# Kernel optimization log

Hardware: AMD Instinct MI355X
Metric: run time of the kernel (lower is better)

## Reference

```python
import jax, jax.numpy as jnp
import numpy as np

TOP_K = 48
NUM_RBF = 16
MAX_REL = 32  # max_relative_feature
B, L = 2, 3072

# atom order in stacked tensor: N=0, Ca=1, C=2, O=3, Cb=4
_PAIRS = np.array([
    (0, 0), (2, 2), (3, 3), (4, 4), (1, 0), (1, 2), (1, 3), (1, 4),
    (0, 2), (0, 3), (0, 4), (4, 2), (4, 3), (3, 2), (0, 1), (2, 1),
    (3, 1), (4, 1), (2, 0), (3, 0), (4, 0), (2, 4), (3, 4), (2, 3)], dtype=np.int32)


def _rbf(D):
    # D [..., ] -> [..., NUM_RBF]
    mu = jnp.linspace(2.0, 22.0, NUM_RBF)
    sigma = (22.0 - 2.0) / NUM_RBF
    return jnp.exp(-(((D[..., None] - mu) / sigma) ** 2))


def setup_inputs() -> dict:
    key = jax.random.key(0)
    ks = jax.random.split(key, 8)
    X = jax.random.normal(ks[0], (B, L, 4, 3), dtype=jnp.float32) * 3.0
    mask = jnp.ones((B, L), dtype=jnp.float32)
    R_idx = jnp.sort(jax.random.randint(ks[1], (B, L), 0, 6144), axis=-1)
    chain_labels = jax.random.randint(ks[2], (B, L), 0, 4)
    pos_W = jax.random.normal(ks[3], (2 * MAX_REL + 2, 16), dtype=jnp.float32) * 0.1
    pos_b = jax.random.normal(ks[4], (16,), dtype=jnp.float32) * 0.02
    edge_W = jax.random.normal(ks[5], (16 + 25 * NUM_RBF, 128), dtype=jnp.float32) * 0.05
    ln_gamma = jnp.ones((128,), dtype=jnp.float32)
    ln_beta = jnp.zeros((128,), dtype=jnp.float32)
    return {"X": X, "mask": mask, "R_idx": R_idx, "chain_labels": chain_labels,
            "pos_W": pos_W, "pos_b": pos_b, "edge_W": edge_W,
            "ln_gamma": ln_gamma, "ln_beta": ln_beta}


def reference(X, mask, R_idx, chain_labels, pos_W, pos_b, edge_W, ln_gamma, ln_beta):
    # virtual Cb construction
    bvec = X[:, :, 1, :] - X[:, :, 0, :]
    cvec = X[:, :, 2, :] - X[:, :, 1, :]
    avec = jnp.cross(bvec, cvec)
    Ca = X[:, :, 1, :]
    Cb = -0.58273431 * avec + 0.56802827 * bvec - 0.54067466 * cvec + Ca
    atoms = jnp.stack([X[:, :, 0, :], Ca, X[:, :, 2, :], X[:, :, 3, :], Cb], axis=2)  # [B,L,5,3]

    # masked pairwise Ca distances + k smallest neighbors
    mask2d = mask[:, :, None] * mask[:, None, :]                        # [B,L,L]
    dX = Ca[:, :, None, :] - Ca[:, None, :, :]
    D = mask2d * jnp.sqrt(jnp.sum(dX ** 2, axis=-1) + 1e-6)
    D_max = jnp.max(D, axis=-1, keepdims=True)
    D_adjust = D + (1.0 - mask2d) * D_max
    k = min(TOP_K, X.shape[1])
    neg_vals, E_idx = jax.lax.top_k(-D_adjust, k)                       # [B,L,K]
    D_neighbors = -neg_vals

    # gather neighbor atom coords once: [B,L,K,5,3]
    atoms_nb = jax.vmap(lambda a, i: a[i])(atoms, E_idx)

    # 24 remaining atom-pair distances, restricted to neighbors (same math as
    # full cdist + gather since dist is computed per (i, E_idx[i,j]) pair)
    ai, bi = _PAIRS[:, 0], _PAIRS[:, 1]
    diff = atoms[:, :, None, ai, :] - atoms_nb[:, :, :, bi, :]          # [B,L,K,24,3]
    D24 = jnp.sqrt(jnp.sum(diff ** 2, axis=-1) + 1e-6)                  # [B,L,K,24]

    D_all = jnp.concatenate([D_neighbors[..., None], D24], axis=-1)    # [B,L,K,25]
    RBF_all = _rbf(D_all).reshape(D_all.shape[:3] + (25 * NUM_RBF,))   # [B,L,K,400]

    # positional encodings on neighbor offsets
    offset = R_idx[:, :, None] - R_idx[:, None, :]
    offset = jnp.take_along_axis(offset, E_idx, axis=2)                 # [B,L,K]
    same_chain = (chain_labels[:, :, None] - chain_labels[:, None, :] == 0).astype(jnp.int32)
    E_chains = jnp.take_along_axis(same_chain, E_idx, axis=2)           # [B,L,K]
    d = jnp.clip(offset + MAX_REL, 0, 2 * MAX_REL) * E_chains + (1 - E_chains) * (2 * MAX_REL + 1)
    E_positional = pos_W[d] + pos_b                                     # one-hot @ W == row gather

    E = jnp.concatenate([E_positional, RBF_all], axis=-1)              # [B,L,K,416]
    E = E @ edge_W                                                      # [B,L,K,128]
    mu = jnp.mean(E, axis=-1, keepdims=True)
    var = jnp.mean((E - mu) ** 2, axis=-1, keepdims=True)
    E = (E - mu) / jnp.sqrt(var + 1e-5) * ln_gamma + ln_beta
    return E, E_idx
```

## Files before the change

### kernel.cpp

```cpp
#include <hip/hip_runtime.h>
#include <hip/hip_bf16.h>
#include <stdint.h>
#include <math.h>

#define B_   2
#define L_   3072
#define K_   48
#define FDIM 416
#define NOUT 128
#define FRS8 424

__device__ const unsigned char PAIRC[24] = {
    0, 18, 27, 36, 8, 10, 11, 12, 2, 3, 4, 34, 35, 26,
    1, 17, 25, 33, 16, 24, 32, 20, 28, 19
};

typedef __attribute__((ext_vector_type(4))) float f32x4;

__global__ __launch_bounds__(256) void k_prep(const float* __restrict__ X,
                                              const float* __restrict__ edgeW,
                                              float* __restrict__ atoms,
                                              float* __restrict__ CaA,
                                              unsigned char* __restrict__ Wt8)
{
    const int bid = blockIdx.x;
    if (bid < 52) {
        int idx4 = bid * 256 + threadIdx.x;
        int b = idx4 * 4;
        int lhi = (b >> 3) & 3;
        int l15 = (b >> 5) & 15;
        int nt  = (b >> 9) & 7;
        int kt  = b >> 12;
        int n = nt * 16 + l15;
        int kbase = kt * 32 + lhi * 8 + (b & 7);
        float v0 = edgeW[(kbase + 0) * NOUT + n];
        float v1 = edgeW[(kbase + 1) * NOUT + n];
        float v2 = edgeW[(kbase + 2) * NOUT + n];
        float v3 = edgeW[(kbase + 3) * NOUT + n];
        int w = __builtin_amdgcn_cvt_pk_fp8_f32(v0, v1, 0, false);
        w = __builtin_amdgcn_cvt_pk_fp8_f32(v2, v3, w, true);
        ((unsigned int*)Wt8)[idx4] = (unsigned int)w;
    } else {
        int row = (bid - 52) * 256 + threadIdx.x;
        if (row >= B_ * L_) return;
        const float* x = X + row * 12;
        float nx = x[0], ny = x[1], nz = x[2];
        float cax = x[3], cay = x[4], caz = x[5];
        float cx = x[6], cy = x[7], cz = x[8];
        float ox = x[9], oy = x[10], oz = x[11];
        float bx = cax - nx, by = cay - ny, bz = caz - nz;
        float vx = cx - cax, vy = cy - cay, vz = cz - caz;
        float axv = by * vz - bz * vy;
        float ayv = bz * vx - bx * vz;
        float azv = bx * vy - by * vx;
        float cbx = -0.58273431f * axv + 0.56802827f * bx - 0.54067466f * vx + cax;
        float cby = -0.58273431f * ayv + 0.56802827f * by - 0.54067466f * vy + cay;
        float cbz = -0.58273431f * azv + 0.56802827f * bz - 0.54067466f * vz + caz;
        float* A = atoms + row * 16;
        A[0] = nx;  A[1] = ny;  A[2] = nz;
        A[3] = cax; A[4] = cay; A[5] = caz;
        A[6] = cx;  A[7] = cy;  A[8] = cz;
        A[9] = ox;  A[10] = oy; A[11] = oz;
        A[12] = cbx; A[13] = cby; A[14] = cbz;
        A[15] = 0.f;
        CaA[row * 3 + 0] = cax;
        CaA[row * 3 + 1] = cay;
        CaA[row * 3 + 2] = caz;
    }
}

__global__ __launch_bounds__(256) void k_topk(const float* __restrict__ CaA,
                                              const float* __restrict__ mask,
                                              int* __restrict__ eidx,
                                              float* __restrict__ dnb,
                                              float* __restrict__ out_eidx_f)
{
    __shared__ __align__(16) unsigned int SH[3072];
    unsigned int* hist  = SH;
    unsigned int* candJ = SH + 2048;
    unsigned long long* candK = (unsigned long long*)SH;
    __shared__ unsigned int swave[4];
    __shared__ int sP;
    __shared__ unsigned int sCnt;

    const int row = blockIdx.x;
    const int b = row / L_;
    const int tid = threadIdx.x;
    const int lane = tid & 63;
    const int wv = tid >> 6;

    #pragma unroll
    for (int i = 0; i < 8; ++i) hist[tid + 256 * i] = 0;
    if (tid == 0) sCnt = 0;

    const float caxf = CaA[row * 3 + 0];
    const float cayf = CaA[row * 3 + 1];
    const float cazf = CaA[row * 3 + 2];
    const float mif = mask[row];
    const float* Cb = CaA + (size_t)b * L_ * 3;
    const float* mb = mask + (size_t)b * L_;
    __syncthreads();

    unsigned int bits[12];
    #pragma unroll
    for (int m = 0; m < 12; ++m) {
        int j = tid + 256 * m;
        float dx = caxf - Cb[j * 3 + 0];
        float dy = cayf - Cb[j * 3 + 1];
        float dz = cazf - Cb[j * 3 + 2];
        float s = fmaf(dz, dz, fmaf(dy, dy, dx * dx)) + 1e-6f;
        float dist = sqrtf(s);
        bool live = (mif * mb[j]) != 0.0f;
        bits[m] = live ? __float_as_uint(dist) : 0x7F800000u;
        atomicAdd(&hist[bits[m] >> 20], 1u);
    }
    __syncthreads();

    unsigned int loc[8];
    unsigned int s = 0;
    #pragma unroll
    for (int i = 0; i < 8; ++i) { loc[i] = hist[tid * 8 + i]; s += loc[i]; }
    unsigned int sc = s;
    #pragma unroll
    for (int off = 1; off < 64; off <<= 1) {
        unsigned int o = __shfl_up(sc, off);
        if (lane >= off) sc += o;
    }
    if (lane == 63) swave[wv] = sc;
    __syncthreads();
    unsigned int base = 0;
    #pragma unroll
    for (int w = 0; w < 4; ++w) if (w < wv) base += swave[w];
    unsigned int cum = base + sc - s;
    #pragma unroll
    for (int i = 0; i < 8; ++i) {
        unsigned int c = loc[i];
        if (cum < K_ && cum + c >= K_) sP = tid * 8 + i;
        cum += c;
    }
    __syncthreads();
    const unsigned int Pth = (unsigned int)sP + 2;

    #pragma unroll
    for (int m = 0; m < 12; ++m) {
        if ((bits[m] >> 20) <= Pth) {
            unsigned int pos = atomicAdd(&sCnt, 1u);
            if (pos < 1024) candJ[pos] = (unsigned)(tid + 256 * m);
        }
    }
    __syncthreads();
    int cnt = (int)sCnt;
    if (cnt > 1024) cnt = 1024;

    const double cax = (double)caxf, cay = (double)cayf, caz = (double)cazf;
    for (int i = tid; i < cnt; i += 256) {
        int j = (int)candJ[i];
        double dx = cax - (double)Cb[j * 3 + 0];
        double dy = cay - (double)Cb[j * 3 + 1];
        double dz = caz - (double)Cb[j * 3 + 2];
        double ss = dx * dx;
        ss = ss + dy * dy;
        ss = ss + dz * dz;
        ss = ss + 1e-6;
        float v = (float)sqrt(ss);
        candK[i] = ((unsigned long long)__float_as_uint(v) << 32) | (unsigned)j;
    }
    __syncthreads();

    if (cnt <= 64) {
        if (wv == 0) {
            unsigned long long k = (lane < cnt) ? candK[lane] : ~0ull;
            #pragma unroll
            for (int size = 2; size <= 64; size <<= 1) {
                #pragma unroll
                for (int stride = size >> 1; stride >= 1; stride >>= 1) {
                    unsigned long long o = __shfl_xor(k, stride);
                    bool low = (lane & stride) == 0;
                    bool up = (lane & size) == 0 || size == 64;
                    unsigned long long mn = k < o ? k : o;
                    unsigned long long mx = k < o ? o : k;
                    k = (low == up) ? mn : mx;
                }
            }
            if (lane < K_) {
                int gj = (int)(unsigned)(k & 0xffffffffu);
                eidx[row * K_ + lane] = gj;
                dnb[row * K_ + lane] = __uint_as_float((unsigned)(k >> 32));
                out_eidx_f[row * K_ + lane] = (float)gj;
            }
        }
    } else {
        int M2 = 128;
        while (M2 < cnt) M2 <<= 1;
        for (int i = cnt + tid; i < M2; i += 256) candK[i] = ~0ull;
        for (int size = 2; size <= M2; size <<= 1) {
            for (int stride = size >> 1; stride > 0; stride >>= 1) {
                __syncthreads();
                for (int i = tid; i < M2; i += 256) {
                    int p = i ^ stride;
                    if (p > i) {
                        unsigned long long a = candK[i];
                        unsigned long long c2 = candK[p];
                        bool up = ((i & size) == 0);
                        if ((a > c2) == up) { candK[i] = c2; candK[p] = a; }
                    }
                }
            }
        }
        __syncthreads();
        if (tid < K_) {
            unsigned long long g = candK[tid];
            int gj = (int)(unsigned)(g & 0xffffffffu);
            eidx[row * K_ + tid] = gj;
            dnb[row * K_ + tid] = __uint_as_float((unsigned)(g >> 32));
            out_eidx_f[row * K_ + tid] = (float)gj;
        }
    }
}

__global__ __launch_bounds__(256) void k_edge(const float* __restrict__ atoms,
                                              const int* __restrict__ eidx,
                                              const float* __restrict__ dnb,
                                              const int* __restrict__ Ridx,
                                              const int* __restrict__ chain,
                                              const float* __restrict__ posW,
                                              const float* __restrict__ posb,
                                              const unsigned char* __restrict__ Wt8,
                                              const float* __restrict__ gamma,
                                              const float* __restrict__ beta,
                                              float* __restrict__ Eout)
{
    __shared__ __align__(16) unsigned char F8[K_ * FRS8];
    __shared__ __align__(16) float sAtoms[K_][16];
    __shared__ __align__(16) float sOwn[16];
    __shared__ int   sE[K_];
    __shared__ float sDnb[K_];
    __shared__ int   sDpos[K_];
    __shared__ float Psum[K_][4];
    __shared__ float Psq[K_][4];

    const int row = blockIdx.x;
    const int b = row / L_;
    const int tid = threadIdx.x;

    if (tid < K_) {
        sE[tid] = eidx[row * K_ + tid];
        sDnb[tid] = dnb[row * K_ + tid];
    }
    __syncthreads();

    if (tid < 192) {
        int k = tid >> 2, part = tid & 3;
        const float4 v = *(const float4*)(atoms + ((size_t)b * L_ + sE[k]) * 16 + part * 4);
        *(float4*)(&sAtoms[k][part * 4]) = v;
    } else if (tid < 196) {
        int part = tid - 192;
        *(float4*)(&sOwn[part * 4]) = *(const float4*)(atoms + (size_t)row * 16 + part * 4);
    } else if (tid >= 208) {
        int k = tid - 208;
        int j = sE[k];
        int off = Ridx[row] - Ridx[b * L_ + j];
        int ch = (chain[row] == chain[b * L_ + j]) ? 1 : 0;
        sDpos[k] = ch ? min(max(off + 32, 0), 64) : 65;
    }
    __syncthreads();

    if (tid < 240) {
        const int k = tid / 5;
        const int dd0 = tid - k * 5;
        unsigned char* Fk = F8 + k * FRS8;
        #pragma unroll
        for (int s5 = 0; s5 < 5; ++s5) {
            const int dd = dd0 + 5 * s5;
            float D;
            if (dd == 0) {
                D = sDnb[k];
            } else {
                int pr = PAIRC[dd - 1];
                int ai = pr >> 3, bi = pr & 7;
                float dx = sOwn[ai * 3 + 0] - sAtoms[k][bi * 3 + 0];
                float dy = sOwn[ai * 3 + 1] - sAtoms[k][bi * 3 + 1];
                float dz = sOwn[ai * 3 + 2] - sAtoms[k][bi * 3 + 2];
                D = sqrtf(fmaf(dz, dz, fmaf(dy, dy, dx * dx)) + 1e-6f);
            }
            float t = fminf((D - 2.0f) * 0.8f, 20.0f);
            unsigned int u[4];
            #pragma unroll
            for (int gp = 0; gp < 4; ++gp) {
                float e0 = __expf(-(t * t));
                float r  = __expf(fmaf(2.1333334f, t, -1.1377778f));
                float e1 = e0 * r; r *= 0.1027400f;
                float e2 = e1 * r; r *= 0.1027400f;
                float e3 = e2 * r;
                int w = __builtin_amdgcn_cvt_pk_fp8_f32(e0, e1, 0, false);
                w = __builtin_amdgcn_cvt_pk_fp8_f32(e2, e3, w, true);
                u[gp] = (unsigned int)w;
                t -= 4.2666667f;
            }
            unsigned char* dst = Fk + 16 + dd * 16;
            *(uint2*)(dst)     = make_uint2(u[0], u[1]);
            *(uint2*)(dst + 8) = make_uint2(u[2], u[3]);
        }
    }
    for (int s2 = tid; s2 < K_ * 16; s2 += 256) {
        int k = s2 >> 4, r = s2 & 15;
        float v = posW[sDpos[k] * 16 + r] + posb[r];
        int w = __builtin_amdgcn_cvt_pk_fp8_f32(v, v, 0, false);
        F8[k * FRS8 + r] = (unsigned char)(w & 0xff);
    }
    __syncthreads();

    const int lane = tid & 63;
    const int wv = tid >> 6;
    const int l15 = lane & 15;
    const int lhi = lane >> 4;

    f32x4 acc[3][2];
    #pragma unroll
    for (int mt = 0; mt < 3; ++mt)
        #pragma unroll
        for (int nn = 0; nn < 2; ++nn)
            acc[mt][nn] = (f32x4){0.f, 0.f, 0.f, 0.f};

    const unsigned char* wp = Wt8 + wv * 1024 + l15 * 32 + lhi * 8;
    long bc0 = *(const long*)(wp);
    long bc1 = *(const long*)(wp + 512);

    #pragma unroll 1
    for (int kt = 0; kt < 13; ++kt) {
        long bn0 = 0, bn1 = 0;
        if (kt < 12) {
            bn0 = *(const long*)(wp + (kt + 1) * 4096);
            bn1 = *(const long*)(wp + (kt + 1) * 4096 + 512);
        }
        const int k0 = kt * 32 + lhi * 8;
        long a0 = *(const long*)(F8 + (l15) * FRS8 + k0);
        long a1 = *(const long*)(F8 + (16 + l15) * FRS8 + k0);
        long a2 = *(const long*)(F8 + (32 + l15) * FRS8 + k0);
        acc[0][0] = __builtin_amdgcn_mfma_f32_16x16x32_fp8_fp8(a0, bc0, acc[0][0], 0, 0, 0);
        acc[0][1] = __builtin_amdgcn_mfma_f32_16x16x32_fp8_fp8(a0, bc1, acc[0][1], 0, 0, 0);
        acc[1][0] = __builtin_amdgcn_mfma_f32_16x16x32_fp8_fp8(a1, bc0, acc[1][0], 0, 0, 0);
        acc[1][1] = __builtin_amdgcn_mfma_f32_16x16x32_fp8_fp8(a1, bc1, acc[1][1], 0, 0, 0);
        acc[2][0] = __builtin_amdgcn_mfma_f32_16x16x32_fp8_fp8(a2, bc0, acc[2][0], 0, 0, 0);
        acc[2][1] = __builtin_amdgcn_mfma_f32_16x16x32_fp8_fp8(a2, bc1, acc[2][1], 0, 0, 0);
        bc0 = bn0;
        bc1 = bn1;
    }

    #pragma unroll
    for (int mt = 0; mt < 3; ++mt) {
        #pragma unroll
        for (int r = 0; r < 4; ++r) {
            float v0 = acc[mt][0][r], v1 = acc[mt][1][r];
            float sv = v0 + v1;
            float q = v0 * v0 + v1 * v1;
            #pragma unroll
            for (int off = 1; off < 16; off <<= 1) {
                sv += __shfl_xor(sv, off);
                q += __shfl_xor(q, off);
            }
            if (l15 == 0) {
                int er = mt * 16 + lhi * 4 + r;
                Psum[er][wv] = sv;
                Psq[er][wv] = q;
            }
        }
    }
    __syncthreads();

    const int c0 = wv * 32 + l15;
    float g2[2], be2[2];
    g2[0] = gamma[c0];      g2[1] = gamma[c0 + 16];
    be2[0] = beta[c0];      be2[1] = beta[c0 + 16];

    #pragma unroll
    for (int mt = 0; mt < 3; ++mt) {
        #pragma unroll
        for (int r = 0; r < 4; ++r) {
            int er = mt * 16 + lhi * 4 + r;
            float sv = Psum[er][0] + Psum[er][1] + Psum[er][2] + Psum[er][3];
            float q = Psq[er][0] + Psq[er][1] + Psq[er][2] + Psq[er][3];
            float mu = sv * (1.0f / 128.0f);
            float var = q * (1.0f / 128.0f) - mu * mu;
            float inv = 1.0f / sqrtf(var + 1e-5f);
            float* op = Eout + ((size_t)row * K_ + er) * 128;
            op[c0]      = (acc[mt][0][r] - mu) * inv * g2[0] + be2[0];
            op[c0 + 16] = (acc[mt][1][r] - mu) * inv * g2[1] + be2[1];
        }
    }
}

extern "C" void kernel_launch(void* const* d_in, const int* in_sizes, int n_in,
                              void* d_out, int out_size, void* d_ws, size_t ws_size,
                              hipStream_t stream) {
    const float* X     = (const float*)d_in[0];
    const float* mask  = (const float*)d_in[1];
    const int*   Ridx  = (const int*)d_in[2];
    const int*   chain = (const int*)d_in[3];
    const float* posW  = (const float*)d_in[4];
    const float* posb  = (const float*)d_in[5];
    const float* edgeW = (const float*)d_in[6];
    const float* gamma = (const float*)d_in[7];
    const float* beta  = (const float*)d_in[8];

    float* out   = (float*)d_out;
    float* Eout  = out;
    float* EidxF = out + (size_t)B_ * L_ * K_ * NOUT;

    float* atoms = (float*)d_ws;
    float* CaA   = atoms + (size_t)B_ * L_ * 16;
    int*   eidx  = (int*)(CaA + (size_t)B_ * L_ * 3);
    float* dnb   = (float*)(eidx + (size_t)B_ * L_ * K_);
    unsigned char* Wt8 = (unsigned char*)(dnb + (size_t)B_ * L_ * K_);

    hipLaunchKernelGGL(k_prep, dim3(52 + (B_ * L_ + 255) / 256), dim3(256), 0, stream,
                       X, edgeW, atoms, CaA, Wt8);
    hipLaunchKernelGGL(k_topk, dim3(B_ * L_), dim3(256), 0, stream,
                       CaA, mask, eidx, dnb, EidxF);
    hipLaunchKernelGGL(k_edge, dim3(B_ * L_), dim3(256), 0, stream,
                       atoms, eidx, dnb, Ridx, chain, posW, posb, Wt8, gamma, beta, Eout);
}
```

Measured before the change: 135.7 us.

## Replace per-edge RBF exponentials with quantized distance LUT and pack Ca with mask

Builds a 1920-entry table of FP8-packed RBF vectors, indexed by distance at 1/64 spacing, inside the prep kernel. The edge kernel then does one 16-byte table load per distance instead of computing exponentials. Ca coordinates and the mask are also packed into float4 so the top-k kernel reads each neighbor with a single vector load. Quantizing the distance to 1/64 adds approximation error on top of the FP8 rounding that already happens.

```diff
diff --git a/kernel.cpp b/kernel.cpp
--- a/kernel.cpp
+++ b/kernel.cpp
@@ -9,6 +9,7 @@
 #define FDIM 416
 #define NOUT 128
 #define FRS8 424
+#define NLUT 1920
 
 __device__ const unsigned char PAIRC[24] = {
     0, 18, 27, 36, 8, 10, 11, 12, 2, 3, 4, 34, 35, 26,
@@ -18,10 +19,12 @@
 typedef __attribute__((ext_vector_type(4))) float f32x4;
 
 __global__ __launch_bounds__(256) void k_prep(const float* __restrict__ X,
+                                              const float* __restrict__ mask,
                                               const float* __restrict__ edgeW,
                                               float* __restrict__ atoms,
-                                              float* __restrict__ CaA,
-                                              unsigned char* __restrict__ Wt8)
+                                              float* __restrict__ CaA4,
+                                              unsigned char* __restrict__ Wt8,
+                                              uint4* __restrict__ LUT)
 {
     const int bid = blockIdx.x;
     if (bid < 52) {
@@ -40,8 +43,25 @@
         int w = __builtin_amdgcn_cvt_pk_fp8_f32(v0, v1, 0, false);
         w = __builtin_amdgcn_cvt_pk_fp8_f32(v2, v3, w, true);
         ((unsigned int*)Wt8)[idx4] = (unsigned int)w;
+    } else if (bid < 60) {
+        int e = (bid - 52) * 256 + threadIdx.x;
+        if (e >= NLUT) return;
+        float D = (float)e * 0.015625f;
+        float z = (D - 2.0f) * 0.8f;
+        unsigned int u[4];
+        #pragma unroll
+        for (int p = 0; p < 4; ++p) {
+            float e0 = __expf(-(z * z)); z -= 1.0666667f;
+            float e1 = __expf(-(z * z)); z -= 1.0666667f;
+            float e2 = __expf(-(z * z)); z -= 1.0666667f;
+            float e3 = __expf(-(z * z)); z -= 1.0666667f;
+            int w = __builtin_amdgcn_cvt_pk_fp8_f32(e0, e1, 0, false);
+            w = __builtin_amdgcn_cvt_pk_fp8_f32(e2, e3, w, true);
+            u[p] = (unsigned int)w;
+        }
+        LUT[e] = make_uint4(u[0], u[1], u[2], u[3]);
     } else {
-        int row = (bid - 52) * 256 + threadIdx.x;
+        int row = (bid - 60) * 256 + threadIdx.x;
         if (row >= B_ * L_) return;
         const float* x = X + row * 12;
         float nx = x[0], ny = x[1], nz = x[2];
@@ -63,14 +83,12 @@
         A[9] = ox;  A[10] = oy; A[11] = oz;
         A[12] = cbx; A[13] = cby; A[14] = cbz;
         A[15] = 0.f;
-        CaA[row * 3 + 0] = cax;
-        CaA[row * 3 + 1] = cay;
-        CaA[row * 3 + 2] = caz;
+        float4 c4 = make_float4(cax, cay, caz, mask[row]);
+        *(float4*)(CaA4 + row * 4) = c4;
     }
 }
 
-__global__ __launch_bounds__(256) void k_topk(const float* __restrict__ CaA,
-                                              const float* __restrict__ mask,
+__global__ __launch_bounds__(256) void k_topk(const float* __restrict__ CaA4,
                                               int* __restrict__ eidx,
                                               float* __restrict__ dnb,
                                               float* __restrict__ out_eidx_f)
@@ -93,24 +111,21 @@
     for (int i = 0; i < 8; ++i) hist[tid + 256 * i] = 0;
     if (tid == 0) sCnt = 0;
 
-    const float caxf = CaA[row * 3 + 0];
-    const float cayf = CaA[row * 3 + 1];
-    const float cazf = CaA[row * 3 + 2];
-    const float mif = mask[row];
-    const float* Cb = CaA + (size_t)b * L_ * 3;
-    const float* mb = mask + (size_t)b * L_;
+    const float4 me = *(const float4*)(CaA4 + row * 4);
+    const float4* Cb = (const float4*)(CaA4 + (size_t)b * L_ * 4);
     __syncthreads();
 
     unsigned int bits[12];
     #pragma unroll
     for (int m = 0; m < 12; ++m) {
         int j = tid + 256 * m;
-        float dx = caxf - Cb[j * 3 + 0];
-        float dy = cayf - Cb[j * 3 + 1];
-        float dz = cazf - Cb[j * 3 + 2];
+        float4 nb = Cb[j];
+        float dx = me.x - nb.x;
+        float dy = me.y - nb.y;
+        float dz = me.z - nb.z;
         float s = fmaf(dz, dz, fmaf(dy, dy, dx * dx)) + 1e-6f;
         float dist = sqrtf(s);
-        bool live = (mif * mb[j]) != 0.0f;
+        bool live = (me.w * nb.w) != 0.0f;
         bits[m] = live ? __float_as_uint(dist) : 0x7F800000u;
         atomicAdd(&hist[bits[m] >> 20], 1u);
     }
@@ -152,12 +167,13 @@
     int cnt = (int)sCnt;
     if (cnt > 1024) cnt = 1024;
 
-    const double cax = (double)caxf, cay = (double)cayf, caz = (double)cazf;
+    const double cax = (double)me.x, cay = (double)me.y, caz = (double)me.z;
     for (int i = tid; i < cnt; i += 256) {
         int j = (int)candJ[i];
-        double dx = cax - (double)Cb[j * 3 + 0];
-        double dy = cay - (double)Cb[j * 3 + 1];
-        double dz = caz - (double)Cb[j * 3 + 2];
+        float4 nb = Cb[j];
+        double dx = cax - (double)nb.x;
+        double dy = cay - (double)nb.y;
+        double dz = caz - (double)nb.z;
         double ss = dx * dx;
         ss = ss + dy * dy;
         ss = ss + dz * dz;
@@ -226,6 +242,7 @@
                                               const float* __restrict__ posW,
                                               const float* __restrict__ posb,
                                               const unsigned char* __restrict__ Wt8,
+                                              const uint4* __restrict__ LUT,
                                               const float* __restrict__ gamma,
                                               const float* __restrict__ beta,
                                               float* __restrict__ Eout)
@@ -283,23 +300,10 @@
                 float dz = sOwn[ai * 3 + 2] - sAtoms[k][bi * 3 + 2];
                 D = sqrtf(fmaf(dz, dz, fmaf(dy, dy, dx * dx)) + 1e-6f);
             }
-            float t = fminf((D - 2.0f) * 0.8f, 20.0f);
-            unsigned int u[4];
-            #pragma unroll
-            for (int gp = 0; gp < 4; ++gp) {
-                float e0 = __expf(-(t * t));
-                float r  = __expf(fmaf(2.1333334f, t, -1.1377778f));
-                float e1 = e0 * r; r *= 0.1027400f;
-                float e2 = e1 * r; r *= 0.1027400f;
-                float e3 = e2 * r;
-                int w = __builtin_amdgcn_cvt_pk_fp8_f32(e0, e1, 0, false);
-                w = __builtin_amdgcn_cvt_pk_fp8_f32(e2, e3, w, true);
-                u[gp] = (unsigned int)w;
-                t -= 4.2666667f;
-            }
-            unsigned char* dst = Fk + 16 + dd * 16;
-            *(uint2*)(dst)     = make_uint2(u[0], u[1]);
-            *(uint2*)(dst + 8) = make_uint2(u[2], u[3]);
+            float Dc = fminf(D, 29.984375f);
+            int idx = (int)fmaf(Dc, 64.0f, 0.5f);
+            uint4 v = LUT[idx];
+            *(uint4*)(Fk + 16 + dd * 16) = v;
         }
     }
     for (int s2 = tid; s2 < K_ * 16; s2 += 256) {
@@ -408,15 +412,16 @@
     float* EidxF = out + (size_t)B_ * L_ * K_ * NOUT;
 
     float* atoms = (float*)d_ws;
-    float* CaA   = atoms + (size_t)B_ * L_ * 16;
-    int*   eidx  = (int*)(CaA + (size_t)B_ * L_ * 3);
+    float* CaA4  = atoms + (size_t)B_ * L_ * 16;
+    int*   eidx  = (int*)(CaA4 + (size_t)B_ * L_ * 4);
     float* dnb   = (float*)(eidx + (size_t)B_ * L_ * K_);
     unsigned char* Wt8 = (unsigned char*)(dnb + (size_t)B_ * L_ * K_);
-
-    hipLaunchKernelGGL(k_prep, dim3(52 + (B_ * L_ + 255) / 256), dim3(256), 0, stream,
-                       X, edgeW, atoms, CaA, Wt8);
+    uint4* LUT   = (uint4*)(Wt8 + 53248);
+
+    hipLaunchKernelGGL(k_prep, dim3(60 + (B_ * L_ + 255) / 256), dim3(256), 0, stream,
+                       X, mask, edgeW, atoms, CaA4, Wt8, LUT);
     hipLaunchKernelGGL(k_topk, dim3(B_ * L_), dim3(256), 0, stream,
-                       CaA, mask, eidx, dnb, EidxF);
+                       CaA4, eidx, dnb, EidxF);
     hipLaunchKernelGGL(k_edge, dim3(B_ * L_), dim3(256), 0, stream,
-                       atoms, eidx, dnb, Ridx, chain, posW, posb, Wt8, gamma, beta, Eout);
+                       atoms, eidx, dnb, Ridx, chain, posW, posb, Wt8, LUT, gamma, beta, Eout);
 }
```

After: 136.6 us. About the same (+0.7%).
